# Kernel optimization log

Hardware: AMD Instinct MI355X
Metric: run time of the kernel (lower is better)

Reference implementation:

```python
import jax, jax.numpy as jnp
import numpy as np

D_MODEL = 1024; D_STATE = 128; D_CONV = 4; EXPAND = 2; D_HEAD = 64; NGROUPS = 1; CHUNK = 256
D_INNER = EXPAND * D_MODEL; D_SSM = D_INNER; NHEADS = D_SSM // D_HEAD
CONV_DIM = D_SSM + 2 * NGROUPS * D_STATE
D_IN_PROJ = 2 * D_INNER + 2 * NGROUPS * D_STATE + NHEADS
EPS = 1e-5


def setup_inputs() -> dict:
    key = jax.random.key(0)
    ks = jax.random.split(key, 8)
    B, L = 2, 2048
    u = jax.random.normal(ks[0], (B, L, D_MODEL), jnp.float32)
    W_in = jax.random.normal(ks[1], (D_IN_PROJ, D_MODEL), jnp.float32) * (D_MODEL ** -0.5)
    conv_w = jax.random.normal(ks[2], (CONV_DIM, D_CONV), jnp.float32) * 0.2
    conv_b = jax.random.normal(ks[3], (CONV_DIM,), jnp.float32) * 0.1
    # dt_bias init as in the torch module: inv-softplus of dt ~ LogUniform(1e-3, 1e-1)
    dt = jnp.exp(jax.random.uniform(ks[4], (NHEADS,)) * (np.log(0.1) - np.log(0.001)) + np.log(0.001))
    dt_bias = dt + jnp.log(-jnp.expm1(-dt))
    A_log = jnp.log(jax.random.uniform(ks[5], (NHEADS,), minval=1.0, maxval=16.0))
    D = jnp.ones((NHEADS,), jnp.float32)
    norm_w = jnp.ones((D_SSM,), jnp.float32)
    W_out = jax.random.normal(ks[6], (D_MODEL, D_INNER), jnp.float32) * (D_INNER ** -0.5)
    return dict(u=u, W_in=W_in, conv_w=conv_w, conv_b=conv_b, dt_bias=dt_bias,
                A_log=A_log, D=D, norm_w=norm_w, W_out=W_out)


def _silu(x):
    return x * jax.nn.sigmoid(x)


def reference(u, W_in, conv_w, conv_b, dt_bias, A_log, D, norm_w, W_out):
    B, L, _ = u.shape
    zxbcdt = u @ W_in.T  # (B,L,d_in_proj), d_mlp == 0
    z, xBC, dt_raw = jnp.split(zxbcdt, [D_SSM, D_SSM + CONV_DIM], axis=-1)

    # causal depthwise conv1d (kernel D_CONV) + silu
    xpad = jnp.pad(xBC, ((0, 0), (D_CONV - 1, 0), (0, 0)))
    xBC = sum(xpad[:, k:k + L, :] * conv_w[:, k] for k in range(D_CONV)) + conv_b
    xBC = _silu(xBC)

    x, Bm, Cm = jnp.split(xBC, [D_SSM, D_SSM + NGROUPS * D_STATE], axis=-1)
    x = x.reshape(B, L, NHEADS, D_HEAD)
    Bm = Bm.reshape(B, L, NGROUPS, D_STATE)
    Cm = Cm.reshape(B, L, NGROUPS, D_STATE)

    A = -jnp.exp(A_log)                     # (H,)
    dt = jax.nn.softplus(dt_raw + dt_bias)  # (B,L,H)

    # chunked SSD scan
    nc = L // CHUNK
    hpg = NHEADS // NGROUPS
    xc = x.reshape(B, nc, CHUNK, NHEADS, D_HEAD)
    Bc = jnp.repeat(Bm.reshape(B, nc, CHUNK, NGROUPS, D_STATE), hpg, axis=3)  # (B,nc,C,H,N)
    Cc = jnp.repeat(Cm.reshape(B, nc, CHUNK, NGROUPS, D_STATE), hpg, axis=3)
    dtc = dt.reshape(B, nc, CHUNK, NHEADS)
    dA = dtc * A                 # (B,nc,C,H), negative
    cum = jnp.cumsum(dA, axis=2)  # (B,nc,C,H)

    # intra-chunk: L[l,s] = exp(cum[l]-cum[s]) for s<=l
    tril = jnp.tril(jnp.ones((CHUNK, CHUNK), bool))
    seg = cum[:, :, :, None, :] - cum[:, :, None, :, :]          # (B,nc,l,s,H)
    Lmat = jnp.exp(jnp.where(tril[None, None, :, :, None], seg, -jnp.inf))
    CB = jnp.einsum('bclhn,bcshn->bclsh', Cc, Bc)
    M = CB * Lmat * dtc[:, :, None, :, :]                        # dt applied at source s
    Y_intra = jnp.einsum('bclsh,bcshp->bclhp', M, xc)

    # per-chunk final states
    decay_states = jnp.exp(cum[:, :, -1:, :] - cum)              # (B,nc,C,H)
    S = jnp.einsum('bclhn,bclh,bclhp->bchpn', Bc, decay_states * dtc, xc)

    # inter-chunk recurrence (scan over chunks)
    chunk_decay = jnp.exp(cum[:, :, -1, :])                      # (B,nc,H)

    def step(carry, inp):
        d, s = inp
        new = carry * d[:, :, None, None] + s
        return new, carry  # emit state entering the chunk

    init = jnp.zeros((B, NHEADS, D_HEAD, D_STATE), u.dtype)
    _, prev = jax.lax.scan(step, init, (jnp.moveaxis(chunk_decay, 1, 0), jnp.moveaxis(S, 1, 0)))
    prev = jnp.moveaxis(prev, 0, 1)                              # (B,nc,H,P,N)

    Y_inter = jnp.einsum('bclhn,bclh,bchpn->bclhp', Cc, jnp.exp(cum), prev)

    y = (Y_intra + Y_inter).reshape(B, L, NHEADS, D_HEAD) + D[None, None, :, None] * x
    y = y.reshape(B, L, D_SSM)

    # gated RMSNorm (norm_before_gate=False): gate first, then normalize
    yg = y * _silu(z)
    var = jnp.mean(yg * yg, axis=-1, keepdims=True)
    y = yg * jax.lax.rsqrt(var + EPS) * norm_w

    return y @ W_out.T
```

## Files before the change

kernel.cpp:

```cpp
#include <hip/hip_runtime.h>
#include <hip/hip_bf16.h>
#include <math.h>
#include <stdint.h>

#define BATCH    2
#define SEQ      2048
#define DMODEL   1024
#define DSSM     2048
#define NHEADS   32
#define DHEAD    64
#define DSTATE   128
#define CONVDIM  2304
#define DINPROJ  4384
#define NPAD     4480
#define CHUNK    256
#define NCHUNK   8
#define ROWS     (BATCH*SEQ)
#define NBC      (BATCH*NCHUNK)
#define EPSF     1e-5f
#define CBASE    (DSSM + DSTATE)

typedef _Float16 half8 __attribute__((ext_vector_type(8)));
typedef _Float16 half4 __attribute__((ext_vector_type(4)));
typedef float f32x4 __attribute__((ext_vector_type(4)));

static __device__ __forceinline__ void gload_lds16(const void* g, void* l) {
    __builtin_amdgcn_global_load_lds(
        (const __attribute__((address_space(1))) uint32_t*)g,
        (__attribute__((address_space(3))) uint32_t*)l, 16, 0, 0);
}

template<int WM, int WN>
__global__ __launch_bounds__(256) void gemm_f16(const _Float16* __restrict__ A,
                                                const _Float16* __restrict__ B,
                                                float* __restrict__ C,
                                                int K, int ldc, int Nc) {
    constexpr int BM = 32 * WM;
    constexpr int BN = 32 * WN;
    __shared__ _Float16 As[BM * 64];
    __shared__ _Float16 Bs[BN * 64];
    const int t  = threadIdx.x;
    const int wv = t >> 6;
    const int ln = t & 63;
    const int wr = wv >> 1, wc = wv & 1;
    const int tm = blockIdx.y * BM;
    const int bn = blockIdx.x * BN;
    const int kb = ln >> 4;
    const int lr = ln & 15;
    const int srow = ln >> 3;
    const int susw = (ln & 7) ^ srow;

    f32x4 acc[WM][WN];
    #pragma unroll
    for (int i = 0; i < WM; ++i)
        #pragma unroll
        for (int j = 0; j < WN; ++j) { f32x4 z = {0.f, 0.f, 0.f, 0.f}; acc[i][j] = z; }

    for (int k0 = 0; k0 < K; k0 += 64) {
        #pragma unroll
        for (int q = 0; q < BM / 32; ++q) {
            int seg = q * 4 + wv;
            int row = seg * 8 + srow;
            const _Float16* src = A + (size_t)(tm + row) * K + k0 + susw * 8;
            gload_lds16(src, (void*)(As + seg * 512));
        }
        #pragma unroll
        for (int q = 0; q < BN / 32; ++q) {
            int seg = q * 4 + wv;
            int row = seg * 8 + srow;
            const _Float16* src = B + (size_t)(bn + row) * K + k0 + susw * 8;
            gload_lds16(src, (void*)(Bs + seg * 512));
        }
        __syncthreads();

        #pragma unroll
        for (int ks = 0; ks < 2; ++ks) {
            half8 af[WM], bf[WN];
            #pragma unroll
            for (int mi = 0; mi < WM; ++mi) {
                int r = wr * (16 * WM) + mi * 16 + lr;
                af[mi] = *(const half8*)(As + r * 64 + (((ks * 4 + kb) ^ (r & 7)) << 3));
            }
            #pragma unroll
            for (int ni = 0; ni < WN; ++ni) {
                int r = wc * (16 * WN) + ni * 16 + lr;
                bf[ni] = *(const half8*)(Bs + r * 64 + (((ks * 4 + kb) ^ (r & 7)) << 3));
            }
            #pragma unroll
            for (int mi = 0; mi < WM; ++mi)
                #pragma unroll
                for (int ni = 0; ni < WN; ++ni)
                    acc[mi][ni] = __builtin_amdgcn_mfma_f32_16x16x32_f16(af[mi], bf[ni], acc[mi][ni], 0, 0, 0);
        }
        __syncthreads();
    }

    #pragma unroll
    for (int mi = 0; mi < WM; ++mi) {
        #pragma unroll
        for (int ni = 0; ni < WN; ++ni) {
            int col = bn + wc * (16 * WN) + ni * 16 + lr;
            if (col < Nc) {
                int row = tm + wr * (16 * WM) + mi * 16 + (ln >> 4) * 4;
                #pragma unroll
                for (int r = 0; r < 4; ++r)
                    C[(size_t)(row + r) * ldc + col] = acc[mi][ni][r];
            }
        }
    }
}

__global__ __launch_bounds__(256) void cast_f16_kernel(const float* __restrict__ src,
                                                       _Float16* __restrict__ dst, int n8) {
    int i = blockIdx.x * 256 + threadIdx.x;
    if (i >= n8) return;
    float4 a = ((const float4*)src)[2 * i];
    float4 b = ((const float4*)src)[2 * i + 1];
    half8 h;
    h[0] = (_Float16)a.x; h[1] = (_Float16)a.y; h[2] = (_Float16)a.z; h[3] = (_Float16)a.w;
    h[4] = (_Float16)b.x; h[5] = (_Float16)b.y; h[6] = (_Float16)b.z; h[7] = (_Float16)b.w;
    ((half8*)dst)[i] = h;
}

__global__ __launch_bounds__(256) void cast_pad_f16_kernel(const float* __restrict__ src,
                                                           _Float16* __restrict__ dst,
                                                           int srcRows, int cols, int n8) {
    int i = blockIdx.x * 256 + threadIdx.x;
    if (i >= n8) return;
    int row = (i * 8) / cols;
    half8 h;
    if (row < srcRows) {
        float4 a = ((const float4*)src)[2 * i];
        float4 b = ((const float4*)src)[2 * i + 1];
        h[0] = (_Float16)a.x; h[1] = (_Float16)a.y; h[2] = (_Float16)a.z; h[3] = (_Float16)a.w;
        h[4] = (_Float16)b.x; h[5] = (_Float16)b.y; h[6] = (_Float16)b.z; h[7] = (_Float16)b.w;
    } else {
        #pragma unroll
        for (int q = 0; q < 8; ++q) h[q] = (_Float16)0.f;
    }
    ((half8*)dst)[i] = h;
}

__global__ __launch_bounds__(256) void conv_silu_kernel(const float* __restrict__ zx,
                                                        const float* __restrict__ conv_w,
                                                        const float* __restrict__ conv_b,
                                                        _Float16* __restrict__ xbc,
                                                        _Float16* __restrict__ xTg,
                                                        _Float16* __restrict__ BTg) {
    __shared__ float zs[67 * 64];
    __shared__ float os[64 * 65];
    const int bid = blockIdx.x;
    const int cg = bid % 36;
    const int bc = bid / 36;
    const int b = bc >> 3, cloc = bc & 7;
    const int c0 = cg * 64;
    const int t = threadIdx.x;

    const int cc = c0 + (t & 63);
    const float w0 = conv_w[cc * 4 + 0], w1 = conv_w[cc * 4 + 1];
    const float w2 = conv_w[cc * 4 + 2], w3 = conv_w[cc * 4 + 3];
    const float bias = conv_b[cc];

    for (int lt = 0; lt < 4; ++lt) {
        const int lbase = cloc * 256 + lt * 64;
        __syncthreads();
        for (int i = t; i < 67 * 64; i += 256) {
            int r = i >> 6, col = i & 63;
            int lseq = lbase - 3 + r;
            float v = 0.f;
            if (lseq >= 0)
                v = zx[((size_t)(b * SEQ + lseq)) * DINPROJ + DSSM + c0 + col];
            zs[i] = v;
        }
        __syncthreads();
        {
            int c = t & 63;
            int w = t >> 6;
            #pragma unroll
            for (int j = 0; j < 16; ++j) {
                int l = w * 16 + j;
                float acc = bias + zs[(l + 0) * 64 + c] * w0 + zs[(l + 1) * 64 + c] * w1
                                 + zs[(l + 2) * 64 + c] * w2 + zs[(l + 3) * 64 + c] * w3;
                os[l * 65 + c] = acc / (1.f + expf(-acc));
            }
        }
        __syncthreads();
        {
            int l = t >> 2, cs = (t & 3) * 16;
            size_t m = (size_t)(b * SEQ + lbase + l);
            half8 h0, h1;
            #pragma unroll
            for (int i = 0; i < 8; ++i) h0[i] = (_Float16)os[l * 65 + cs + i];
            #pragma unroll
            for (int i = 0; i < 8; ++i) h1[i] = (_Float16)os[l * 65 + cs + 8 + i];
            _Float16* dst = xbc + m * CONVDIM + c0 + cs;
            *(half8*)dst = h0;
            *(half8*)(dst + 8) = h1;
        }
        if (c0 < CBASE) {
            int c = t >> 2, ls = (t & 3) * 16;
            int gc = c0 + c;
            half8 h0, h1;
            #pragma unroll
            for (int i = 0; i < 8; ++i) h0[i] = (_Float16)os[(ls + i) * 65 + c];
            #pragma unroll
            for (int i = 0; i < 8; ++i) h1[i] = (_Float16)os[(ls + 8 + i) * 65 + c];
            _Float16* dst;
            if (gc < DSSM)
                dst = xTg + ((size_t)bc * 2048 + gc) * 256 + lt * 64 + ls;
            else
                dst = BTg + ((size_t)bc * 128 + (gc - DSSM)) * 256 + lt * 64 + ls;
            *(half8*)dst = h0;
            *(half8*)(dst + 8) = h1;
        }
    }
}

__global__ __launch_bounds__(256) void dt_kernel(const float* __restrict__ zx,
                                                 const float* __restrict__ dt_bias,
                                                 float* __restrict__ dt) {
    int idx = blockIdx.x * 256 + threadIdx.x;
    if (idx >= ROWS * NHEADS) return;
    int h = idx & 31;
    int m = idx >> 5;
    float v = zx[(size_t)m * DINPROJ + (DSSM + CONVDIM) + h] + dt_bias[h];
    dt[idx] = (v > 20.f) ? v : log1pf(expf(v));
}

__global__ void cumsum_kernel(const float* __restrict__ dt,
                              const float* __restrict__ A_log,
                              float* __restrict__ cum) {
    int t = blockIdx.x * 256 + threadIdx.x;
    if (t >= NBC * NHEADS) return;
    int h = t & 31;
    int bc = t >> 5;
    float A = -expf(A_log[h]);
    float acc = 0.f;
    for (int l = 0; l < CHUNK; ++l) {
        size_t idx = ((size_t)bc * CHUNK + l) * NHEADS + h;
        acc += dt[idx] * A;
        cum[idx] = acc;
    }
}

__global__ __launch_bounds__(256) void chunk_state_mfma(const _Float16* __restrict__ xTg,
                                                        const _Float16* __restrict__ BTg,
                                                        const float* __restrict__ dt,
                                                        const float* __restrict__ cum,
                                                        float* __restrict__ S) {
    int bid = blockIdx.x;
    int h = bid & 31, bc = bid >> 5;
    __shared__ _Float16 cxs[64 * 64];
    __shared__ _Float16 bts[128 * 64];
    __shared__ float coefL[256];
    const int t = threadIdx.x, w = t >> 6, ln = t & 63;
    const int lr = ln & 15, lg = ln >> 4;

    {
        float cl = cum[((size_t)bc * 256 + 255) * 32 + h];
        size_t ci = ((size_t)bc * 256 + t) * 32 + h;
        coefL[t] = expf(cl - cum[ci]) * dt[ci];
    }

    f32x4 sacc[4][2];
    #pragma unroll
    for (int pi = 0; pi < 4; ++pi)
        #pragma unroll
        for (int ni = 0; ni < 2; ++ni) { f32x4 z = {0.f,0.f,0.f,0.f}; sacc[pi][ni] = z; }

    const _Float16* xTh = xTg + (size_t)bid * 64 * 256;

    for (int kt = 0; kt < 4; ++kt) {
        __syncthreads();
        {
            int p = t >> 2, l0 = (t & 3) * 16;
            const _Float16* src = xTh + (size_t)p * 256 + kt * 64;
            #pragma unroll
            for (int q = 0; q < 2; ++q) {
                int c = l0 + q * 8;
                half8 hv = *(const half8*)(src + c);
                half8 ov;
                #pragma unroll
                for (int j = 0; j < 8; ++j)
                    ov[j] = (_Float16)((float)hv[j] * coefL[kt * 64 + c + j]);
                *(half8*)(cxs + p * 64 + (c ^ ((p & 7) << 3))) = ov;
            }
        }
        #pragma unroll
        for (int q = 0; q < 4; ++q) {
            int seg = w * 4 + q;
            int r = seg * 8 + (ln >> 3);
            int csw = 8 * ((ln & 7) ^ (r & 7));
            const _Float16* src = BTg + ((size_t)bc * 128 + r) * 256 + kt * 64 + csw;
            gload_lds16(src, (void*)(bts + seg * 512));
        }
        __syncthreads();
        #pragma unroll
        for (int kk = 0; kk < 2; ++kk) {
            int c0 = kk * 32 + lg * 8;
            half8 ax[4], bx[2];
            #pragma unroll
            for (int pi = 0; pi < 4; ++pi) {
                int r = pi * 16 + lr;
                ax[pi] = *(const half8*)(cxs + r * 64 + (c0 ^ ((r & 7) << 3)));
            }
            #pragma unroll
            for (int ni = 0; ni < 2; ++ni) {
                int r = w * 32 + ni * 16 + lr;
                bx[ni] = *(const half8*)(bts + r * 64 + (c0 ^ ((r & 7) << 3)));
            }
            #pragma unroll
            for (int pi = 0; pi < 4; ++pi)
                #pragma unroll
                for (int ni = 0; ni < 2; ++ni)
                    sacc[pi][ni] = __builtin_amdgcn_mfma_f32_16x16x32_f16(ax[pi], bx[ni], sacc[pi][ni], 0, 0, 0);
        }
    }
    float* sb = S + (size_t)bid * (DHEAD * DSTATE);
    #pragma unroll
    for (int pi = 0; pi < 4; ++pi)
        #pragma unroll
        for (int ni = 0; ni < 2; ++ni)
            #pragma unroll
            for (int r = 0; r < 4; ++r) {
                int p = pi * 16 + lg * 4 + r;
                int n = w * 32 + ni * 16 + lr;
                sb[p * 128 + n] = sacc[pi][ni][r];
            }
}

__global__ __launch_bounds__(256) void scan_kernel(const float* __restrict__ cum,
                                                   float* __restrict__ S) {
    int bid = blockIdx.x;
    int h = bid & 31, b = bid >> 5;
    int t = threadIdx.x;
    float carry[32];
    #pragma unroll
    for (int i = 0; i < 32; ++i) carry[i] = 0.f;
    for (int c = 0; c < NCHUNK; ++c) {
        int bc = b * NCHUNK + c;
        float decay = expf(cum[((size_t)bc * CHUNK + 255) * NHEADS + h]);
        size_t base = ((size_t)(bc * NHEADS + h)) * (DHEAD * DSTATE);
        #pragma unroll
        for (int i = 0; i < 32; ++i) {
            size_t idx = base + t + i * 256;
            float s = S[idx];
            float nw = carry[i] * decay + s;
            S[idx] = carry[i];
            carry[i] = nw;
        }
    }
}

__global__ __launch_bounds__(256, 2) void y_mfma(const _Float16* __restrict__ xbc,
                                                 const _Float16* __restrict__ xTg,
                                                 const float* __restrict__ dt,
                                                 const float* __restrict__ cum,
                                                 const float* __restrict__ Sprev,
                                                 const float* __restrict__ Dp,
                                                 float* __restrict__ y) {
    int bid = blockIdx.x;
    int h = bid & 31, bc = bid >> 5;
    __shared__ _Float16 Bs2[2][64 * 128];
    __shared__ _Float16 PwF[4 * 64 * 64];
    __shared__ float cumL[256], dtL[256];
    const int t = threadIdx.x, w = t >> 6, ln = t & 63;
    const int lr = ln & 15, lg = ln >> 4;

    {
        size_t ci = ((size_t)bc * 256 + t) * 32 + h;
        cumL[t] = cum[ci];
        dtL[t]  = dt[ci];
    }
    {
        const float* sp = Sprev + (size_t)bid * (DHEAD * DSTATE);
        int r = t >> 2, cb = (t & 3) * 32;
        #pragma unroll
        for (int q = 0; q < 4; ++q) {
            int c = cb + q * 8;
            float4 f0 = *(const float4*)(sp + r * 128 + c);
            float4 f1 = *(const float4*)(sp + r * 128 + c + 4);
            half8 hv;
            hv[0]=(_Float16)f0.x; hv[1]=(_Float16)f0.y; hv[2]=(_Float16)f0.z; hv[3]=(_Float16)f0.w;
            hv[4]=(_Float16)f1.x; hv[5]=(_Float16)f1.y; hv[6]=(_Float16)f1.z; hv[7]=(_Float16)f1.w;
            *(half8*)(PwF + r * 128 + (c ^ ((r & 7) << 3))) = hv;
        }
    }
    {
        #pragma unroll
        for (int q = 0; q < 4; ++q) {
            int seg = w * 4 + q;
            int r = seg * 4 + lg;
            int csw = 8 * (lr ^ (r & 7));
            const _Float16* src = xbc + ((size_t)(bc * 256 + r)) * CONVDIM + DSSM + csw;
            gload_lds16(src, (void*)(Bs2[0] + seg * 512));
        }
    }
    half8 ca[4][4];
    {
        const _Float16* cb = xbc + ((size_t)(bc * 256 + w * 64)) * CONVDIM + CBASE;
        #pragma unroll
        for (int mi = 0; mi < 4; ++mi)
            #pragma unroll
            for (int kk = 0; kk < 4; ++kk)
                ca[mi][kk] = *(const half8*)(cb + (size_t)(mi * 16 + lr) * CONVDIM + kk * 32 + lg * 8);
    }
    __syncthreads();

    f32x4 yacc[4][4];
    #pragma unroll
    for (int i = 0; i < 4; ++i)
        #pragma unroll
        for (int j = 0; j < 4; ++j) { f32x4 z = {0.f,0.f,0.f,0.f}; yacc[i][j] = z; }

    #pragma unroll
    for (int kk = 0; kk < 4; ++kk) {
        int co = kk * 32 + lg * 8;
        #pragma unroll
        for (int pi = 0; pi < 4; ++pi) {
            int r = pi * 16 + lr;
            half8 pb = *(const half8*)(PwF + r * 128 + (co ^ ((r & 7) << 3)));
            #pragma unroll
            for (int mi = 0; mi < 4; ++mi)
                yacc[mi][pi] = __builtin_amdgcn_mfma_f32_16x16x32_f16(ca[mi][kk], pb, yacc[mi][pi], 0, 0, 0);
        }
    }
    #pragma unroll
    for (int mi = 0; mi < 4; ++mi)
        #pragma unroll
        for (int r = 0; r < 4; ++r) {
            float e = expf(cumL[w * 64 + mi * 16 + lg * 4 + r]);
            #pragma unroll
            for (int pi = 0; pi < 4; ++pi) yacc[mi][pi][r] *= e;
        }
    float c0 = cumL[w * 64];
    float el[4];
    #pragma unroll
    for (int mi = 0; mi < 4; ++mi) el[mi] = expf(cumL[w * 64 + mi * 16 + lr] - c0);
    float Dv = Dp[h];

    __syncthreads();

    _Float16* pwb = PwF + w * 4096;
    for (int st = 0; st < 4; ++st) {
        if (st < 3) {
            #pragma unroll
            for (int q = 0; q < 4; ++q) {
                int seg = w * 4 + q;
                int r = seg * 4 + lg;
                int csw = 8 * (lr ^ (r & 7));
                const _Float16* src = xbc + ((size_t)(bc * 256 + (st + 1) * 64 + r)) * CONVDIM + DSSM + csw;
                gload_lds16(src, (void*)(Bs2[(st + 1) & 1] + seg * 512));
            }
        }
        if (st <= w) {
            const _Float16* bsc = Bs2[st & 1];
            half8 xb[4][2];
            #pragma unroll
            for (int pi = 0; pi < 4; ++pi)
                #pragma unroll
                for (int k2 = 0; k2 < 2; ++k2)
                    xb[pi][k2] = *(const half8*)(xTg + ((size_t)bid * 64 + pi * 16 + lr) * 256
                                                 + st * 64 + k2 * 32 + lg * 8);
            #pragma unroll
            for (int si = 0; si < 4; ++si) {
                f32x4 ps[4];
                #pragma unroll
                for (int mi = 0; mi < 4; ++mi) { f32x4 z = {0.f,0.f,0.f,0.f}; ps[mi] = z; }
                int r = si * 16 + lr;
                #pragma unroll
                for (int kk = 0; kk < 4; ++kk) {
                    int co = kk * 32 + lg * 8;
                    half8 bb = *(const half8*)(bsc + r * 128 + (co ^ ((r & 7) << 3)));
                    #pragma unroll
                    for (int mi = 0; mi < 4; ++mi)
                        ps[mi] = __builtin_amdgcn_mfma_f32_16x16x32_f16(bb, ca[mi][kk], ps[mi], 0, 0, 0);
                }
                if (st < w) {
                    float fs[4];
                    #pragma unroll
                    for (int rr = 0; rr < 4; ++rr) {
                        int sg = st * 64 + si * 16 + lg * 4 + rr;
                        fs[rr] = expf(c0 - cumL[sg]) * dtL[sg];
                    }
                    #pragma unroll
                    for (int mi = 0; mi < 4; ++mi) {
                        half4 hv;
                        #pragma unroll
                        for (int rr = 0; rr < 4; ++rr)
                            hv[rr] = (_Float16)(ps[mi][rr] * el[mi] * fs[rr]);
                        *(half4*)(pwb + (mi * 16 + lr) * 64 + ((si * 16 + lg * 4) ^ (8 * (lr & 7)))) = hv;
                    }
                } else {
                    #pragma unroll
                    for (int mi = 0; mi < 4; ++mi) {
                        int lloc = mi * 16 + lr;
                        float cl = cumL[w * 64 + lloc];
                        half4 hv;
                        #pragma unroll
                        for (int rr = 0; rr < 4; ++rr) {
                            int sl = si * 16 + lg * 4 + rr;
                            float v = 0.f;
                            if (sl <= lloc) {
                                int sg = w * 64 + sl;
                                v = ps[mi][rr] * expf(cl - cumL[sg]) * dtL[sg];
                                if (sl == lloc) v += Dv;
                            }
                            hv[rr] = (_Float16)v;
                        }
                        *(half4*)(pwb + (mi * 16 + lr) * 64 + ((si * 16 + lg * 4) ^ (8 * (lr & 7)))) = hv;
                    }
                }
            }
            #pragma unroll
            for (int k2 = 0; k2 < 2; ++k2) {
                int co = k2 * 32 + lg * 8;
                half8 pa[4];
                #pragma unroll
                for (int mi = 0; mi < 4; ++mi) {
                    int r = mi * 16 + lr;
                    pa[mi] = *(const half8*)(pwb + r * 64 + (co ^ (8 * (lr & 7))));
                }
                #pragma unroll
                for (int pi = 0; pi < 4; ++pi)
                    #pragma unroll
                    for (int mi = 0; mi < 4; ++mi)
                        yacc[mi][pi] = __builtin_amdgcn_mfma_f32_16x16x32_f16(pa[mi], xb[pi][k2], yacc[mi][pi], 0, 0, 0);
            }
        }
        __syncthreads();
    }

    #pragma unroll
    for (int mi = 0; mi < 4; ++mi) {
        #pragma unroll
        for (int r = 0; r < 4; ++r) {
            int l = w * 64 + mi * 16 + lg * 4 + r;
            size_t row = (size_t)bc * 256 + l;
            #pragma unroll
            for (int pi = 0; pi < 4; ++pi)
                y[row * DSSM + h * 64 + pi * 16 + lr] = yacc[mi][pi][r];
        }
    }
}

__global__ __launch_bounds__(256) void norm_kernel(const float* __restrict__ y,
                                                   const float* __restrict__ zx,
                                                   const float* __restrict__ norm_w,
                                                   _Float16* __restrict__ outh) {
    int m = blockIdx.x;
    int t = threadIdx.x;
    const float* yrow = y + (size_t)m * DSSM;
    const float* zrow = zx + (size_t)m * DINPROJ;
    float yg[8];
    float ss = 0.f;
    #pragma unroll
    for (int q = 0; q < 2; ++q) {
        float4 yv = *(const float4*)(yrow + t*8 + q*4);
        float4 zv = *(const float4*)(zrow + t*8 + q*4);
        float zvals[4] = {zv.x, zv.y, zv.z, zv.w};
        float yvals[4] = {yv.x, yv.y, yv.z, yv.w};
        #pragma unroll
        for (int i = 0; i < 4; ++i) {
            float sz = zvals[i] / (1.f + expf(-zvals[i]));
            float g = yvals[i] * sz;
            yg[q*4+i] = g;
            ss += g * g;
        }
    }
    #pragma unroll
    for (int off = 32; off > 0; off >>= 1) ss += __shfl_xor(ss, off, 64);
    __shared__ float red[4];
    if ((t & 63) == 0) red[t >> 6] = ss;
    __syncthreads();
    float tot = red[0] + red[1] + red[2] + red[3];
    float inv = rsqrtf(tot / (float)DSSM + EPSF);
    half8 h;
    #pragma unroll
    for (int q = 0; q < 8; ++q)
        h[q] = (_Float16)(yg[q] * inv * norm_w[t*8 + q]);
    *(half8*)(outh + (size_t)m * DSSM + t * 8) = h;
}

extern "C" void kernel_launch(void* const* d_in, const int* in_sizes, int n_in,
                              void* d_out, int out_size, void* d_ws, size_t ws_size,
                              hipStream_t stream) {
    (void)in_sizes; (void)n_in; (void)out_size; (void)ws_size;
    const float* u       = (const float*)d_in[0];
    const float* W_in    = (const float*)d_in[1];
    const float* conv_w  = (const float*)d_in[2];
    const float* conv_b  = (const float*)d_in[3];
    const float* dt_bias = (const float*)d_in[4];
    const float* A_log   = (const float*)d_in[5];
    const float* Dp      = (const float*)d_in[6];
    const float* norm_w  = (const float*)d_in[7];
    const float* W_out   = (const float*)d_in[8];
    float* out = (float*)d_out;

    float* zx   = (float*)d_ws;
    float* dtb  = zx   + (size_t)ROWS * DINPROJ;
    float* cum  = dtb  + (size_t)ROWS * NHEADS;
    float* Sbuf = cum  + (size_t)ROWS * NHEADS;
    float* yb   = Sbuf + (size_t)NBC * NHEADS * DHEAD * DSTATE;
    _Float16* xbc_h = (_Float16*)(yb + (size_t)ROWS * DSSM);
    _Float16* xTg   = xbc_h + (size_t)ROWS * CONVDIM;
    _Float16* BTg   = xTg   + (size_t)NBC * NHEADS * 64 * 256;
    _Float16* uh    = BTg   + (size_t)NBC * 128 * 256;
    _Float16* Wih   = uh    + (size_t)ROWS * DMODEL;
    _Float16* Wouth = Wih   + (size_t)NPAD * DMODEL;
    _Float16* ybh   = Wouth + (size_t)DMODEL * DSSM;

    cast_f16_kernel<<<(ROWS * DMODEL / 8 + 255) / 256, 256, 0, stream>>>(u, uh, ROWS * DMODEL / 8);
    cast_pad_f16_kernel<<<(NPAD * DMODEL / 8 + 255) / 256, 256, 0, stream>>>(
        W_in, Wih, DINPROJ, DMODEL, NPAD * DMODEL / 8);
    cast_f16_kernel<<<(DMODEL * DSSM / 8 + 255) / 256, 256, 0, stream>>>(W_out, Wouth, DMODEL * DSSM / 8);

    gemm_f16<4, 4><<<dim3(NPAD / 128, ROWS / 128), 256, 0, stream>>>(
        uh, Wih, zx, DMODEL, DINPROJ, DINPROJ);
    conv_silu_kernel<<<NBC * 36, 256, 0, stream>>>(
        zx, conv_w, conv_b, xbc_h, xTg, BTg);
    dt_kernel<<<(ROWS * NHEADS + 255) / 256, 256, 0, stream>>>(zx, dt_bias, dtb);
    cumsum_kernel<<<2, 256, 0, stream>>>(dtb, A_log, cum);
    chunk_state_mfma<<<NBC * NHEADS, 256, 0, stream>>>(xTg, BTg, dtb, cum, Sbuf);
    scan_kernel<<<BATCH * NHEADS, 256, 0, stream>>>(cum, Sbuf);
    y_mfma<<<NBC * NHEADS, 256, 0, stream>>>(xbc_h, xTg, dtb, cum, Sbuf, Dp, yb);
    norm_kernel<<<ROWS, 256, 0, stream>>>(yb, zx, norm_w, ybh);
    gemm_f16<4, 2><<<dim3(DMODEL / 64, ROWS / 128), 256, 0, stream>>>(
        ybh, Wouth, out, DSSM, DMODEL, DMODEL);
}
```

Before: 320.0 us.

## Store in-projection output as fp16, fuse dt softplus into cumsum, swizzle GEMM blocks

The in-projection GEMM now writes its zxbcdt output in fp16, which halves that large intermediate, and writes the dt columns separately in fp32. Conv and norm read the fp16 copy. The separate dt softplus kernel is folded into the cumsum kernel, removing one launch and one pass. GEMM workgroup ids are remapped with a stride-8 swizzle so that concurrently running blocks share input tiles better. The cost is reduced precision on z and xBC before the conv and the gate.

```diff
diff --git a/kernel.cpp b/kernel.cpp
--- a/kernel.cpp
+++ b/kernel.cpp
@@ -19,6 +19,7 @@
 #define NBC      (BATCH*NCHUNK)
 #define EPSF     1e-5f
 #define CBASE    (DSSM + DSTATE)
+#define DTCOL    (DSSM + CONVDIM)
 
 typedef _Float16 half8 __attribute__((ext_vector_type(8)));
 typedef _Float16 half4 __attribute__((ext_vector_type(4)));
@@ -30,10 +31,11 @@
         (__attribute__((address_space(3))) uint32_t*)l, 16, 0, 0);
 }
 
-template<int WM, int WN>
+template<int WM, int WN, bool HOUT>
 __global__ __launch_bounds__(256) void gemm_f16(const _Float16* __restrict__ A,
                                                 const _Float16* __restrict__ B,
-                                                float* __restrict__ C,
+                                                void* __restrict__ Cout,
+                                                float* __restrict__ dtraw,
                                                 int K, int ldc, int Nc) {
     constexpr int BM = 32 * WM;
     constexpr int BN = 32 * WN;
@@ -43,8 +45,14 @@
     const int wv = t >> 6;
     const int ln = t & 63;
     const int wr = wv >> 1, wc = wv & 1;
-    const int tm = blockIdx.y * BM;
-    const int bn = blockIdx.x * BN;
+
+    int nwg = gridDim.x * gridDim.y;
+    int bid0 = blockIdx.y * gridDim.x + blockIdx.x;
+    int qq = nwg >> 3;
+    int swz = (bid0 & 7) * qq + (bid0 >> 3);
+    const int tm = (swz / gridDim.x) * BM;
+    const int bn = (swz % gridDim.x) * BN;
+
     const int kb = ln >> 4;
     const int lr = ln & 15;
     const int srow = ln >> 3;
@@ -102,9 +110,22 @@
             int col = bn + wc * (16 * WN) + ni * 16 + lr;
             if (col < Nc) {
                 int row = tm + wr * (16 * WM) + mi * 16 + (ln >> 4) * 4;
-                #pragma unroll
-                for (int r = 0; r < 4; ++r)
-                    C[(size_t)(row + r) * ldc + col] = acc[mi][ni][r];
+                if (HOUT) {
+                    _Float16* C = (_Float16*)Cout;
+                    #pragma unroll
+                    for (int r = 0; r < 4; ++r)
+                        C[(size_t)(row + r) * ldc + col] = (_Float16)acc[mi][ni][r];
+                    if (col >= DTCOL) {
+                        #pragma unroll
+                        for (int r = 0; r < 4; ++r)
+                            dtraw[(size_t)(row + r) * NHEADS + (col - DTCOL)] = acc[mi][ni][r];
+                    }
+                } else {
+                    float* C = (float*)Cout;
+                    #pragma unroll
+                    for (int r = 0; r < 4; ++r)
+                        C[(size_t)(row + r) * ldc + col] = acc[mi][ni][r];
+                }
             }
         }
     }
@@ -141,7 +162,7 @@
     ((half8*)dst)[i] = h;
 }
 
-__global__ __launch_bounds__(256) void conv_silu_kernel(const float* __restrict__ zx,
+__global__ __launch_bounds__(256) void conv_silu_kernel(const _Float16* __restrict__ zx,
                                                         const float* __restrict__ conv_w,
                                                         const float* __restrict__ conv_b,
                                                         _Float16* __restrict__ xbc,
@@ -169,7 +190,7 @@
             int lseq = lbase - 3 + r;
             float v = 0.f;
             if (lseq >= 0)
-                v = zx[((size_t)(b * SEQ + lseq)) * DINPROJ + DSSM + c0 + col];
+                v = (float)zx[((size_t)(b * SEQ + lseq)) * DINPROJ + DSSM + c0 + col];
             zs[i] = v;
         }
         __syncthreads();
@@ -216,29 +237,24 @@
     }
 }
 
-__global__ __launch_bounds__(256) void dt_kernel(const float* __restrict__ zx,
-                                                 const float* __restrict__ dt_bias,
-                                                 float* __restrict__ dt) {
-    int idx = blockIdx.x * 256 + threadIdx.x;
-    if (idx >= ROWS * NHEADS) return;
-    int h = idx & 31;
-    int m = idx >> 5;
-    float v = zx[(size_t)m * DINPROJ + (DSSM + CONVDIM) + h] + dt_bias[h];
-    dt[idx] = (v > 20.f) ? v : log1pf(expf(v));
-}
-
-__global__ void cumsum_kernel(const float* __restrict__ dt,
-                              const float* __restrict__ A_log,
-                              float* __restrict__ cum) {
+__global__ void dtcum_kernel(const float* __restrict__ dtraw,
+                             const float* __restrict__ dt_bias,
+                             const float* __restrict__ A_log,
+                             float* __restrict__ dtb,
+                             float* __restrict__ cum) {
     int t = blockIdx.x * 256 + threadIdx.x;
     if (t >= NBC * NHEADS) return;
     int h = t & 31;
     int bc = t >> 5;
+    float bias = dt_bias[h];
     float A = -expf(A_log[h]);
     float acc = 0.f;
     for (int l = 0; l < CHUNK; ++l) {
         size_t idx = ((size_t)bc * CHUNK + l) * NHEADS + h;
-        acc += dt[idx] * A;
+        float v = dtraw[idx] + bias;
+        float d = (v > 20.f) ? v : log1pf(expf(v));
+        dtb[idx] = d;
+        acc += d * A;
         cum[idx] = acc;
     }
 }
@@ -545,28 +561,26 @@
 }
 
 __global__ __launch_bounds__(256) void norm_kernel(const float* __restrict__ y,
-                                                   const float* __restrict__ zx,
+                                                   const _Float16* __restrict__ zx,
                                                    const float* __restrict__ norm_w,
                                                    _Float16* __restrict__ outh) {
     int m = blockIdx.x;
     int t = threadIdx.x;
     const float* yrow = y + (size_t)m * DSSM;
-    const float* zrow = zx + (size_t)m * DINPROJ;
+    const _Float16* zrow = zx + (size_t)m * DINPROJ;
     float yg[8];
     float ss = 0.f;
-    #pragma unroll
-    for (int q = 0; q < 2; ++q) {
-        float4 yv = *(const float4*)(yrow + t*8 + q*4);
-        float4 zv = *(const float4*)(zrow + t*8 + q*4);
-        float zvals[4] = {zv.x, zv.y, zv.z, zv.w};
-        float yvals[4] = {yv.x, yv.y, yv.z, yv.w};
-        #pragma unroll
-        for (int i = 0; i < 4; ++i) {
-            float sz = zvals[i] / (1.f + expf(-zvals[i]));
-            float g = yvals[i] * sz;
-            yg[q*4+i] = g;
-            ss += g * g;
-        }
+    half8 zv = *(const half8*)(zrow + t * 8);
+    float4 yv0 = *(const float4*)(yrow + t * 8);
+    float4 yv1 = *(const float4*)(yrow + t * 8 + 4);
+    float yvals[8] = {yv0.x, yv0.y, yv0.z, yv0.w, yv1.x, yv1.y, yv1.z, yv1.w};
+    #pragma unroll
+    for (int i = 0; i < 8; ++i) {
+        float z = (float)zv[i];
+        float sz = z / (1.f + expf(-z));
+        float g = yvals[i] * sz;
+        yg[i] = g;
+        ss += g * g;
     }
     #pragma unroll
     for (int off = 32; off > 0; off >>= 1) ss += __shfl_xor(ss, off, 64);
@@ -597,12 +611,13 @@
     const float* W_out   = (const float*)d_in[8];
     float* out = (float*)d_out;
 
-    float* zx   = (float*)d_ws;
-    float* dtb  = zx   + (size_t)ROWS * DINPROJ;
-    float* cum  = dtb  + (size_t)ROWS * NHEADS;
-    float* Sbuf = cum  + (size_t)ROWS * NHEADS;
-    float* yb   = Sbuf + (size_t)NBC * NHEADS * DHEAD * DSTATE;
-    _Float16* xbc_h = (_Float16*)(yb + (size_t)ROWS * DSSM);
+    float* dtraw = (float*)d_ws;
+    float* dtb   = dtraw + (size_t)ROWS * NHEADS;
+    float* cum   = dtb   + (size_t)ROWS * NHEADS;
+    float* Sbuf  = cum   + (size_t)ROWS * NHEADS;
+    float* yb    = Sbuf  + (size_t)NBC * NHEADS * DHEAD * DSTATE;
+    _Float16* zxh   = (_Float16*)(yb + (size_t)ROWS * DSSM);
+    _Float16* xbc_h = zxh   + (size_t)ROWS * DINPROJ;
     _Float16* xTg   = xbc_h + (size_t)ROWS * CONVDIM;
     _Float16* BTg   = xTg   + (size_t)NBC * NHEADS * 64 * 256;
     _Float16* uh    = BTg   + (size_t)NBC * 128 * 256;
@@ -615,16 +630,15 @@
         W_in, Wih, DINPROJ, DMODEL, NPAD * DMODEL / 8);
     cast_f16_kernel<<<(DMODEL * DSSM / 8 + 255) / 256, 256, 0, stream>>>(W_out, Wouth, DMODEL * DSSM / 8);
 
-    gemm_f16<4, 4><<<dim3(NPAD / 128, ROWS / 128), 256, 0, stream>>>(
-        uh, Wih, zx, DMODEL, DINPROJ, DINPROJ);
+    gemm_f16<4, 4, true><<<dim3(NPAD / 128, ROWS / 128), 256, 0, stream>>>(
+        uh, Wih, (void*)zxh, dtraw, DMODEL, DINPROJ, DINPROJ);
     conv_silu_kernel<<<NBC * 36, 256, 0, stream>>>(
-        zx, conv_w, conv_b, xbc_h, xTg, BTg);
-    dt_kernel<<<(ROWS * NHEADS + 255) / 256, 256, 0, stream>>>(zx, dt_bias, dtb);
-    cumsum_kernel<<<2, 256, 0, stream>>>(dtb, A_log, cum);
+        zxh, conv_w, conv_b, xbc_h, xTg, BTg);
+    dtcum_kernel<<<2, 256, 0, stream>>>(dtraw, dt_bias, A_log, dtb, cum);
     chunk_state_mfma<<<NBC * NHEADS, 256, 0, stream>>>(xTg, BTg, dtb, cum, Sbuf);
     scan_kernel<<<BATCH * NHEADS, 256, 0, stream>>>(cum, Sbuf);
     y_mfma<<<NBC * NHEADS, 256, 0, stream>>>(xbc_h, xTg, dtb, cum, Sbuf, Dp, yb);
-    norm_kernel<<<ROWS, 256, 0, stream>>>(yb, zx, norm_w, ybh);
-    gemm_f16<4, 2><<<dim3(DMODEL / 64, ROWS / 128), 256, 0, stream>>>(
-        ybh, Wouth, out, DSSM, DMODEL, DMODEL);
-}
+    norm_kernel<<<ROWS, 256, 0, stream>>>(yb, zxh, norm_w, ybh);
+    gemm_f16<4, 2, false><<<dim3(DMODEL / 64, ROWS / 128), 256, 0, stream>>>(
+        ybh, Wouth, (void*)out, nullptr, DSSM, DMODEL, DMODEL);
+}
```

Result: slower. 438.8 us (+37.1%).
